# Performance work log

Measured on AMD Instinct MI355X. Metric: run time of the kernel, lower is better.

## Reference

```python
import jax, jax.numpy as jnp
import numpy as np
from jax import lax

BN_EPS = 1e-5


def ternarize(w):
    """Per-output-channel ternary quantization (Li & Liu TWN style).
    delta_i = 0.7 * mean(|w_i|); alpha_i = mean of |w| over entries with |w| > delta_i;
    output = alpha_i * (+1 where w > delta_i, -1 where w < -delta_i, else 0).
    """
    aw = jnp.abs(w)
    axes = tuple(range(1, w.ndim))
    delta = 0.7 * jnp.mean(aw, axis=axes)            # [O]
    d = delta.reshape((-1,) + (1,) * (w.ndim - 1))   # broadcastable
    mask = aw > d
    alpha = jnp.sum(aw * mask, axis=axes) / jnp.sum(mask, axis=axes)
    tern = jnp.where(w > d, 1.0, 0.0) - jnp.where(w < -d, 1.0, 0.0)
    return tern * alpha.reshape(d.shape)


def batchnorm2d(x, gamma, beta):
    # training-mode batchnorm: batch statistics over (N, H, W), biased variance
    mean = jnp.mean(x, axis=(0, 2, 3), keepdims=True)
    var = jnp.mean((x - mean) ** 2, axis=(0, 2, 3), keepdims=True)
    xhat = (x - mean) * lax.rsqrt(var + BN_EPS)
    return xhat * gamma[None, :, None, None] + beta[None, :, None, None]


def conv2d(x, w, b):
    out = lax.conv_general_dilated(x, w, window_strides=(1, 1), padding='VALID',
                                   dimension_numbers=('NCHW', 'OIHW', 'NCHW'))
    return out + b[None, :, None, None]


def maxpool2(x):
    return lax.reduce_window(x, -jnp.inf, lax.max, (1, 1, 2, 2), (1, 1, 2, 2), 'VALID')


def setup_inputs() -> dict:
    key = jax.random.key(0)
    ks = jax.random.split(key, 10)
    B = 4096
    return {
        'x': jax.random.normal(ks[0], (B, 1, 28, 28), jnp.float32),
        'w_conv1': jax.random.normal(ks[1], (32, 1, 5, 5), jnp.float32) * 0.2,
        'b_conv1': jax.random.normal(ks[2], (32,), jnp.float32) * 0.1,
        'gamma1': jnp.ones((32,), jnp.float32),
        'beta1': jnp.zeros((32,), jnp.float32),
        'w_conv2': jax.random.normal(ks[3], (64, 32, 5, 5), jnp.float32) * 0.05,
        'b_conv2': jax.random.normal(ks[4], (64,), jnp.float32) * 0.1,
        'gamma2': jnp.ones((64,), jnp.float32),
        'beta2': jnp.zeros((64,), jnp.float32),
        'w_fc1': jax.random.normal(ks[5], (512, 1024), jnp.float32) * 0.03,
        'b_fc1': jax.random.normal(ks[6], (512,), jnp.float32) * 0.1,
        'w_fc2': jax.random.normal(ks[7], (10, 512), jnp.float32) * 0.05,
        'b_fc2': jax.random.normal(ks[8], (10,), jnp.float32) * 0.1,
    }


def reference(x, w_conv1, b_conv1, gamma1, beta1, w_conv2, b_conv2, gamma2, beta2,
              w_fc1, b_fc1, w_fc2, b_fc2):
    h = conv2d(x, ternarize(w_conv1), b_conv1)          # [B,32,24,24]
    h = jax.nn.relu(maxpool2(batchnorm2d(h, gamma1, beta1)))  # [B,32,12,12]
    h = conv2d(h, ternarize(w_conv2), b_conv2)          # [B,64,8,8]
    h = jax.nn.relu(maxpool2(batchnorm2d(h, gamma2, beta2)))  # [B,64,4,4]
    h = h.reshape(-1, 1024)
    h = jax.nn.relu(h @ ternarize(w_fc1).T + b_fc1)     # [B,512]
    return h @ ternarize(w_fc2).T + b_fc2               # [B,10]
```

## Files before the change

kernel.cpp:

```cpp
#include <hip/hip_runtime.h>

#define TID ((int)threadIdx.x)
typedef unsigned short ushort_t;
typedef short short8 __attribute__((ext_vector_type(8)));
typedef float f32x4 __attribute__((ext_vector_type(4)));

__device__ __forceinline__ float bf2f(ushort_t u) {
    return __uint_as_float(((unsigned int)u) << 16);
}
__device__ __forceinline__ ushort_t f2bf(float f) {
    unsigned int x = __float_as_uint(f);
    return (ushort_t)((x + 0x7FFFu + ((x >> 16) & 1u)) >> 16);
}
__device__ __forceinline__ float ld1(const void* p, int i, bool f32) {
    return f32 ? ((const float*)p)[i] : bf2f(((const ushort_t*)p)[i]);
}
__device__ __forceinline__ bool probe_f32(const void* g1) {
    return ((const ushort_t*)g1)[0] == 0x0000u;
}
__device__ __forceinline__ short8 bn8relu(short8 u, float a, float h) {
    short8 r;
#pragma unroll
    for (int j = 0; j < 8; ++j) {
        float v = bf2f((ushort_t)u[j]);
        r[j] = (short)f2bf(fmaxf(fmaf(a, v, h), 0.f));
    }
    return r;
}

__global__ __launch_bounds__(256) void tern_pack_kernel(
    const void* __restrict__ w1, const void* __restrict__ w2,
    const void* __restrict__ wf1, const void* __restrict__ wf2,
    ushort_t* __restrict__ wpack1, ushort_t* __restrict__ wpack2,
    ushort_t* __restrict__ wf1pack, ushort_t* __restrict__ wf2pack,
    float* __restrict__ stats_z, const void* __restrict__ g1probe)
{
    const bool f32 = probe_f32(g1probe);
    const int blk = blockIdx.x;
    if (blk < 48) stats_z[blk * 256 + TID] = 0.f;

    const void* w; int K, o, seg;
    if (blk < 32)       { w = w1;  K = 25;   o = blk;       seg = 0; }
    else if (blk < 96)  { w = w2;  K = 800;  o = blk - 32;  seg = 1; }
    else if (blk < 608) { w = wf1; K = 1024; o = blk - 96;  seg = 2; }
    else                { w = wf2; K = 512;  o = blk - 608; seg = 3; }

    const size_t base = (size_t)o * K;
    __shared__ float redA[4], redB[4], redC[4];
    const int lane = TID & 63, wv = TID >> 6;

    float wreg[4];
#pragma unroll
    for (int t = 0; t < 4; ++t) {
        const int k = t * 256 + TID;
        wreg[t] = (k < K) ? ld1(w, base + k, f32) : 0.f;
    }

    float s = fabsf(wreg[0]) + fabsf(wreg[1]) + fabsf(wreg[2]) + fabsf(wreg[3]);
#pragma unroll
    for (int d = 1; d < 64; d <<= 1) s += __shfl_xor(s, d);
    if (lane == 0) redA[wv] = s;
    __syncthreads();
    const float delta = 0.7f * (redA[0] + redA[1] + redA[2] + redA[3]) / (float)K;

    float ms = 0.f, cnt = 0.f;
#pragma unroll
    for (int t = 0; t < 4; ++t) {
        float aw = fabsf(wreg[t]);
        if (aw > delta) { ms += aw; cnt += 1.f; }
    }
#pragma unroll
    for (int d = 1; d < 64; d <<= 1) {
        ms += __shfl_xor(ms, d);
        cnt += __shfl_xor(cnt, d);
    }
    if (lane == 0) { redB[wv] = ms; redC[wv] = cnt; }
    __syncthreads();
    const float denom = redC[0] + redC[1] + redC[2] + redC[3];
    const float alpha = (denom > 0.f)
        ? ((redB[0] + redB[1] + redB[2] + redB[3]) / denom) : 0.f;

#pragma unroll
    for (int t = 0; t < 4; ++t) {
        const int k = t * 256 + TID;
        if (k >= K) break;
        float v = wreg[t];
        ushort_t tb = f2bf((v > delta) ? alpha : ((v < -delta) ? -alpha : 0.f));
        if (seg == 0) {
            const int kp = (k / 5) * 6 + (k % 5);
            wpack1[((size_t)(o >> 4) * 64 + (kp >> 3) * 16 + (o & 15)) * 8 + (kp & 7)] = tb;
        } else if (seg == 1) {
            const int pos = k % 25, ic = k / 25;
            wpack2[((size_t)(pos * 4 + (o >> 4)) * 64 + (ic >> 3) * 16 + (o & 15)) * 8
                   + (ic & 7)] = tb;
        } else if (seg == 2) {
            wf1pack[((size_t)((k >> 5) * 32 + (o >> 4)) * 64 + ((k >> 3) & 3) * 16
                     + (o & 15)) * 8 + (k & 7)] = tb;
        } else {
            wf2pack[((size_t)(k >> 5) * 64 + ((k >> 3) & 3) * 16 + o) * 8 + (k & 7)] = tb;
        }
    }
    if (seg == 0 && TID < 7) {
        const int kps[7] = {5, 11, 17, 23, 29, 30, 31};
        const int kp = kps[TID];
        wpack1[((size_t)(o >> 4) * 64 + (kp >> 3) * 16 + (o & 15)) * 8 + (kp & 7)] = 0;
    }
}

__device__ __forceinline__ void conv1_koff(int qd, int* koff) {
#pragma unroll
    for (int j = 0; j < 8; ++j) {
        int k = qd * 8 + j, ky = k / 6, kx = k - ky * 6;
        koff[j] = (k < 30 && kx < 5) ? (ky * 28 + kx) : -1;
    }
}

__global__ __launch_bounds__(256) void conv1_stats_kernel(
    const void* __restrict__ x, const ushort_t* __restrict__ wpack1u,
    const void* __restrict__ gamma1, float* __restrict__ stats,
    ushort_t* __restrict__ pooled1)
{
    const bool f32 = probe_f32(gamma1);
    const short8* wpack1 = (const short8*)wpack1u;
    __shared__ uint xsI[784];
    __shared__ float reds[4][64];
    const int b0 = blockIdx.x * 2;
    if (TID < 196) {
        uint4 u;
        if (f32) {
            float4 v0 = ((const float4*)x)[(size_t)b0 * 196 + TID];
            float4 v1 = ((const float4*)x)[(size_t)(b0 + 1) * 196 + TID];
            u.x = (uint)f2bf(v0.x) | ((uint)f2bf(v1.x) << 16);
            u.y = (uint)f2bf(v0.y) | ((uint)f2bf(v1.y) << 16);
            u.z = (uint)f2bf(v0.z) | ((uint)f2bf(v1.z) << 16);
            u.w = (uint)f2bf(v0.w) | ((uint)f2bf(v1.w) << 16);
        } else {
            ushort4 u0 = ((const ushort4*)x)[(size_t)b0 * 196 + TID];
            ushort4 u1 = ((const ushort4*)x)[(size_t)(b0 + 1) * 196 + TID];
            u.x = (uint)u0.x | ((uint)u1.x << 16);
            u.y = (uint)u0.y | ((uint)u1.y << 16);
            u.z = (uint)u0.z | ((uint)u1.z << 16);
            u.w = (uint)u0.w | ((uint)u1.w << 16);
        }
        *(uint4*)&xsI[TID * 4] = u;
    }
    __syncthreads();

    const int lane = TID & 63, wv = TID >> 6;
    const int qd = lane >> 4, ln15 = lane & 15;
    int koff[8];
    conv1_koff(qd, koff);
    const short8 bw0 = wpack1[lane];
    const short8 bw1 = wpack1[64 + lane];
    const bool pos0 = ld1(gamma1, ln15, f32) >= 0.f;
    const bool pos1 = ld1(gamma1, 16 + ln15, f32) >= 0.f;

    float s0 = 0.f, q0 = 0.f, s1 = 0.f, q1 = 0.f;
    const int cellA0 = (ln15 >> 2);
    const int m3 = ln15 & 3;
    const size_t pbA = (size_t)b0 * 144;
    const size_t pbB = (size_t)(b0 + 1) * 144;
    for (int t = wv * 9; t < wv * 9 + 9; ++t) {
        const int cellA = t * 4 + cellA0;
        const int pbase = ((cellA / 12) * 2 + (m3 >> 1)) * 28
                        + (cellA % 12) * 2 + (m3 & 1);
        uint g[8];
#pragma unroll
        for (int j = 0; j < 8; ++j)
            g[j] = (koff[j] >= 0) ? xsI[pbase + koff[j]] : 0u;
        short8 a0, a1;
#pragma unroll
        for (int j = 0; j < 8; ++j) {
            a0[j] = (short)(g[j] & 0xFFFFu);
            a1[j] = (short)(g[j] >> 16);
        }
        f32x4 c00 = {0.f,0.f,0.f,0.f}, c01 = {0.f,0.f,0.f,0.f};
        f32x4 c10 = {0.f,0.f,0.f,0.f}, c11 = {0.f,0.f,0.f,0.f};
        c00 = __builtin_amdgcn_mfma_f32_16x16x32_bf16(a0, bw0, c00, 0, 0, 0);
        c01 = __builtin_amdgcn_mfma_f32_16x16x32_bf16(a0, bw1, c01, 0, 0, 0);
        c10 = __builtin_amdgcn_mfma_f32_16x16x32_bf16(a1, bw0, c10, 0, 0, 0);
        c11 = __builtin_amdgcn_mfma_f32_16x16x32_bf16(a1, bw1, c11, 0, 0, 0);
#pragma unroll
        for (int r = 0; r < 4; ++r) {
            s0 += c00[r] + c10[r]; q0 += c00[r]*c00[r] + c10[r]*c10[r];
            s1 += c01[r] + c11[r]; q1 += c01[r]*c01[r] + c11[r]*c11[r];
        }
        const int cell = t * 4 + qd;
        float mxA0 = fmaxf(fmaxf(c00[0], c00[1]), fmaxf(c00[2], c00[3]));
        float mnA0 = fminf(fminf(c00[0], c00[1]), fminf(c00[2], c00[3]));
        float mxA1 = fmaxf(fmaxf(c01[0], c01[1]), fmaxf(c01[2], c01[3]));
        float mnA1 = fminf(fminf(c01[0], c01[1]), fminf(c01[2], c01[3]));
        pooled1[(pbA + cell) * 32 + ln15]      = f2bf(pos0 ? mxA0 : mnA0);
        pooled1[(pbA + cell) * 32 + 16 + ln15] = f2bf(pos1 ? mxA1 : mnA1);
        float mxB0 = fmaxf(fmaxf(c10[0], c10[1]), fmaxf(c10[2], c10[3]));
        float mnB0 = fminf(fminf(c10[0], c10[1]), fminf(c10[2], c10[3]));
        float mxB1 = fmaxf(fmaxf(c11[0], c11[1]), fmaxf(c11[2], c11[3]));
        float mnB1 = fminf(fminf(c11[0], c11[1]), fminf(c11[2], c11[3]));
        pooled1[(pbB + cell) * 32 + ln15]      = f2bf(pos0 ? mxB0 : mnB0);
        pooled1[(pbB + cell) * 32 + 16 + ln15] = f2bf(pos1 ? mxB1 : mnB1);
    }
    s0 += __shfl_xor(s0, 16); q0 += __shfl_xor(q0, 16);
    s1 += __shfl_xor(s1, 16); q1 += __shfl_xor(q1, 16);
    s0 += __shfl_xor(s0, 32); q0 += __shfl_xor(q0, 32);
    s1 += __shfl_xor(s1, 32); q1 += __shfl_xor(q1, 32);
    if (lane < 16) {
        reds[wv][ln15]      = s0;
        reds[wv][32 + ln15] = q0;
        reds[wv][16 + ln15] = s1;
        reds[wv][48 + ln15] = q1;
    }
    __syncthreads();
    if (TID < 64) {
        float v = reds[0][TID] + reds[1][TID] + reds[2][TID] + reds[3][TID];
        atomicAdd(&stats[(blockIdx.x & 63) * 64 + TID], v);
    }
}

__global__ __launch_bounds__(256) void conv12_kernel(
    const ushort_t* __restrict__ pooled1, const float* __restrict__ stats,
    const void* __restrict__ gamma1, const void* __restrict__ beta1,
    const ushort_t* __restrict__ wpack2u,
    const void* __restrict__ b2, const void* __restrict__ gamma2,
    ushort_t* __restrict__ pooled2, float* __restrict__ stats2)
{
    const bool f32 = probe_f32(gamma1);
    const short8* wpack2 = (const short8*)wpack2u;
    __shared__ ushort_t p1b[2][144 * 40];
    __shared__ float r2[4][64];
    __shared__ float as1[32], hs1[32];
    const int b0 = blockIdx.x * 2;

    {
        const int c = TID & 63, g = TID >> 6;
        float v = 0.f;
        for (int sl = g; sl < 64; sl += 4) v += stats[sl * 64 + c];
        r2[g][c] = v;
    }
    __syncthreads();
    if (TID < 32) {
        float s = r2[0][TID] + r2[1][TID] + r2[2][TID] + r2[3][TID];
        float q = r2[0][32 + TID] + r2[1][32 + TID]
                + r2[2][32 + TID] + r2[3][32 + TID];
        const float invN = 1.f / 2359296.f;
        float mraw = s * invN;
        float var  = q * invN - mraw * mraw;
        float rstd = rsqrtf(fmaxf(var, 0.f) + 1e-5f);
        float g1v = ld1(gamma1, TID, f32) * rstd;
        as1[TID] = g1v;
        hs1[TID] = ld1(beta1, TID, f32) - mraw * g1v;
    }
    __syncthreads();

    {
        const uint* pm = (const uint*)(pooled1 + (size_t)b0 * 4608);
        const int ch2 = (TID & 15) * 2;
        const float aA = as1[ch2],     hA = hs1[ch2];
        const float aB = as1[ch2 + 1], hB = hs1[ch2 + 1];
#pragma unroll
        for (int i = 0; i < 18; ++i) {
            const int idx = i * 256 + TID;
            const int img = (idx >= 2304) ? 1 : 0;
            const int cell = (idx - img * 2304) >> 4;
            const uint u = pm[idx];
            float v0 = bf2f((ushort_t)(u & 0xFFFFu));
            float v1 = bf2f((ushort_t)(u >> 16));
            uint o0 = f2bf(fmaxf(fmaf(aA, v0, hA), 0.f));
            uint o1 = f2bf(fmaxf(fmaf(aB, v1, hB), 0.f));
            *(uint*)&p1b[img][cell * 40 + ch2] = o0 | (o1 << 16);
        }
    }
    __syncthreads();

    const int lane = TID & 63, wv = TID >> 6;
    const int qd = lane >> 4, ln15 = lane & 15;
    const int mh = wv >> 1, nh = wv & 1;
    const int px0 = (mh * 2 + 0) * 16 + ln15;
    const int px1 = (mh * 2 + 1) * 16 + ln15;
    const int base0 = (px0 >> 3) * 12 + (px0 & 7);
    const int base1 = (px1 >> 3) * 12 + (px1 & 7);

    f32x4 acc[2][2][2] = {};
#pragma unroll
    for (int pos = 0; pos < 25; ++pos) {
        const int koff2 = (pos / 5) * 12 + (pos % 5);
        short8 bb0 = wpack2[(pos * 4 + nh * 2 + 0) * 64 + lane];
        short8 bb1 = wpack2[(pos * 4 + nh * 2 + 1) * 64 + lane];
#pragma unroll
        for (int img = 0; img < 2; ++img) {
            short8 a0 = *(const short8*)&p1b[img][(base0 + koff2) * 40 + qd * 8];
            short8 a1 = *(const short8*)&p1b[img][(base1 + koff2) * 40 + qd * 8];
            acc[img][0][0] = __builtin_amdgcn_mfma_f32_16x16x32_bf16(a0, bb0, acc[img][0][0], 0, 0, 0);
            acc[img][0][1] = __builtin_amdgcn_mfma_f32_16x16x32_bf16(a0, bb1, acc[img][0][1], 0, 0, 0);
            acc[img][1][0] = __builtin_amdgcn_mfma_f32_16x16x32_bf16(a1, bb0, acc[img][1][0], 0, 0, 0);
            acc[img][1][1] = __builtin_amdgcn_mfma_f32_16x16x32_bf16(a1, bb1, acc[img][1][1], 0, 0, 0);
        }
    }

#pragma unroll
    for (int jn = 0; jn < 2; ++jn) {
        const int oc = (nh * 2 + jn) * 16 + ln15;
        const float bias = ld1(b2, oc, f32);
        const bool gpos = ld1(gamma2, oc, f32) >= 0.f;
        float s0 = 0.f, q0 = 0.f;
#pragma unroll
        for (int img = 0; img < 2; ++img) {
            const size_t p2base = (size_t)(b0 + img) * 1024;
#pragma unroll
            for (int i = 0; i < 2; ++i) {
                float v0 = acc[img][i][jn][0] + bias;
                float v1 = acc[img][i][jn][1] + bias;
                float v2 = acc[img][i][jn][2] + bias;
                float v3 = acc[img][i][jn][3] + bias;
                s0 += v0 + v1 + v2 + v3;
                q0 += v0*v0 + v1*v1 + v2*v2 + v3*v3;
                float mx01 = fmaxf(v0, v1), mn01 = fminf(v0, v1);
                float mx23 = fmaxf(v2, v3), mn23 = fminf(v2, v3);
                mx01 = fmaxf(mx01, __shfl_xor(mx01, 32));
                mn01 = fminf(mn01, __shfl_xor(mn01, 32));
                mx23 = fmaxf(mx23, __shfl_xor(mx23, 32));
                mn23 = fminf(mn23, __shfl_xor(mn23, 32));
                if (qd < 2) {
                    ushort2 st;
                    st.x = f2bf(gpos ? mx01 : mn01);
                    st.y = f2bf(gpos ? mx23 : mn23);
                    const int ti = mh * 2 + i;
                    *(ushort2*)&pooled2[p2base + (size_t)oc * 16 + ti * 4 + 2 * qd] = st;
                }
            }
        }
        s0 += __shfl_down(s0, 32); q0 += __shfl_down(q0, 32);
        s0 += __shfl_down(s0, 16); q0 += __shfl_down(q0, 16);
        if (lane < 16) {
            r2[wv][jn * 32 + lane]      = s0;
            r2[wv][jn * 32 + 16 + lane] = q0;
        }
    }
    __syncthreads();
    if (TID < 128) {
        const int idx = TID & 63, nh2 = TID >> 6;
        float v = r2[nh2][idx] + r2[nh2 + 2][idx];
        const int jn = idx >> 5, isq = (idx >> 4) & 1, chx = idx & 15;
        const int oc = nh2 * 32 + jn * 16 + chx;
        atomicAdd(&stats2[(blockIdx.x & 63) * 128 + isq * 64 + oc], v);
    }
}

__global__ __launch_bounds__(256) void fc1_kernel(
    const ushort_t* __restrict__ A, const ushort_t* __restrict__ wf1packu,
    const float* __restrict__ stats2,
    const void* __restrict__ gamma2, const void* __restrict__ beta2,
    const void* __restrict__ bias, ushort_t* __restrict__ out,
    const void* __restrict__ g1probe)
{
    const bool f32 = probe_f32(g1probe);
    const short8* wf1pack = (const short8*)wf1packu;
    __shared__ float bn2[2][128];
    __shared__ float a2s[64], h2s[64];
    const int m0 = blockIdx.y * 64;
    const int n0x4 = blockIdx.x * 4;
    const int lane = TID & 63;
    const int wv   = TID >> 6;
    const int mh = wv >> 1, nh = wv & 1;
    const int qd = lane >> 4, ln15 = lane & 15;

    {
        const int c = TID & 127, g = TID >> 7;
        float v = 0.f;
        for (int sl = g; sl < 64; sl += 2) v += stats2[sl * 128 + c];
        bn2[g][c] = v;
    }
    __syncthreads();
    if (TID < 64) {
        float s = bn2[0][TID] + bn2[1][TID];
        float q = bn2[0][64 + TID] + bn2[1][64 + TID];
        const float invN = 1.f / 262144.f;
        float mean = s * invN;
        float var  = q * invN - mean * mean;
        float rstd = rsqrtf(fmaxf(var, 0.f) + 1e-5f);
        float g2 = ld1(gamma2, TID, f32) * rstd;
        a2s[TID] = g2;
        h2s[TID] = ld1(beta2, TID, f32) - mean * g2;
    }
    __syncthreads();

    const ushort_t* arow0 = A + (size_t)(m0 + mh * 32 + ln15) * 1024 + qd * 8;
    const ushort_t* arow1 = arow0 + 16 * 1024;

    f32x4 acc[2][2] = {};
#pragma unroll 8
    for (int kk = 0; kk < 32; ++kk) {
        const int oc = kk * 2 + (qd >> 1);
        const float a2 = a2s[oc], h2 = h2s[oc];
        short8 a0 = bn8relu(*(const short8*)(arow0 + kk * 32), a2, h2);
        short8 a1 = bn8relu(*(const short8*)(arow1 + kk * 32), a2, h2);
        short8 bb0 = wf1pack[(kk * 32 + n0x4 + nh * 2 + 0) * 64 + lane];
        short8 bb1 = wf1pack[(kk * 32 + n0x4 + nh * 2 + 1) * 64 + lane];
        acc[0][0] = __builtin_amdgcn_mfma_f32_16x16x32_bf16(a0, bb0, acc[0][0], 0, 0, 0);
        acc[0][1] = __builtin_amdgcn_mfma_f32_16x16x32_bf16(a0, bb1, acc[0][1], 0, 0, 0);
        acc[1][0] = __builtin_amdgcn_mfma_f32_16x16x32_bf16(a1, bb0, acc[1][0], 0, 0, 0);
        acc[1][1] = __builtin_amdgcn_mfma_f32_16x16x32_bf16(a1, bb1, acc[1][1], 0, 0, 0);
    }

#pragma unroll
    for (int jn = 0; jn < 2; ++jn) {
        const int n = n0x4 * 16 + (nh * 2 + jn) * 16 + ln15;
        const float bv = ld1(bias, n, f32);
#pragma unroll
        for (int i = 0; i < 2; ++i) {
            const int mb = m0 + (mh * 2 + i) * 16 + qd * 4;
#pragma unroll
            for (int r = 0; r < 4; ++r) {
                float v = fmaxf(acc[i][jn][r] + bv, 0.f);
                out[(size_t)(mb + r) * 512 + n] = f2bf(v);
            }
        }
    }
}

__global__ __launch_bounds__(256) void fc2_kernel(
    const ushort_t* __restrict__ h, const ushort_t* __restrict__ wf2packu,
    const void* __restrict__ bias, void* __restrict__ out,
    const void* __restrict__ g1probe)
{
    const bool f32 = probe_f32(g1probe);
    const short8* wf2pack = (const short8*)wf2packu;
    const int lane = TID & 63, wv = TID >> 6;
    const int qd = lane >> 4, ln15 = lane & 15;
    const int m0 = (blockIdx.x * 4 + wv) * 16;

    f32x4 acc = {0.f, 0.f, 0.f, 0.f};
#pragma unroll
    for (int kk = 0; kk < 16; ++kk) {
        short8 a = *(const short8*)&h[(size_t)(m0 + ln15) * 512 + kk * 32 + qd * 8];
        acc = __builtin_amdgcn_mfma_f32_16x16x32_bf16(a, wf2pack[kk * 64 + lane],
                                                      acc, 0, 0, 0);
    }
    if (ln15 < 10) {
        const float bv = ld1(bias, ln15, f32);
#pragma unroll
        for (int r = 0; r < 4; ++r) {
            const size_t oi = (size_t)(m0 + qd * 4 + r) * 10 + ln15;
            float v = acc[r] + bv;
            if (f32) ((float*)out)[oi] = v;
            else ((ushort_t*)out)[oi] = f2bf(v);
        }
    }
}

extern "C" void kernel_launch(void* const* d_in, const int* in_sizes, int n_in,
                              void* d_out, int out_size, void* d_ws, size_t ws_size,
                              hipStream_t stream)
{
    const void* x       = d_in[0];
    const void* w_conv1 = d_in[1];
    const void* gamma1  = d_in[3];
    const void* beta1   = d_in[4];
    const void* w_conv2 = d_in[5];
    const void* b_conv2 = d_in[6];
    const void* gamma2  = d_in[7];
    const void* beta2   = d_in[8];
    const void* w_fc1   = d_in[9];
    const void* b_fc1   = d_in[10];
    const void* w_fc2   = d_in[11];
    const void* b_fc2   = d_in[12];

    char* wsb = (char*)d_ws;
    size_t off = 0;
    auto alloc = [&](size_t bytes) -> void* {
        void* p = wsb + off;
        off += (bytes + 255) & ~(size_t)255;
        return p;
    };

    float*    stats   = (float*)alloc(49152);
    float*    stats2  = stats + 4096;
    ushort_t* wpack1  = (ushort_t*)alloc(2 * 64 * 16);
    ushort_t* wpack2  = (ushort_t*)alloc(25 * 4 * 64 * 16);
    ushort_t* wf1pack = (ushort_t*)alloc((size_t)32 * 32 * 64 * 16);
    ushort_t* wf2pack = (ushort_t*)alloc(16 * 64 * 16);
    ushort_t* pooled1 = (ushort_t*)alloc((size_t)4096 * 144 * 32 * 2);
    ushort_t* pooled2 = (ushort_t*)alloc((size_t)4096 * 64 * 16 * 2);
    ushort_t* fc1o    = (ushort_t*)alloc((size_t)4096 * 512 * 2);

    tern_pack_kernel<<<618, 256, 0, stream>>>(w_conv1, w_conv2, w_fc1, w_fc2,
                                              wpack1, wpack2, wf1pack, wf2pack,
                                              stats, gamma1);

    conv1_stats_kernel<<<2048, 256, 0, stream>>>(x, wpack1, gamma1,
                                                 stats, pooled1);

    conv12_kernel<<<2048, 256, 0, stream>>>(pooled1, stats, gamma1, beta1,
                                            wpack2, b_conv2, gamma2,
                                            pooled2, stats2);

    fc1_kernel<<<dim3(8, 64), 256, 0, stream>>>(pooled2, wf1pack, stats2,
                                                gamma2, beta2, b_fc1,
                                                fc1o, gamma1);
    fc2_kernel<<<64, 256, 0, stream>>>(fc1o, wf2pack, b_fc2, d_out, gamma1);
}
```

Before: 182.2 us.

## Recompute conv1 in conv2 kernel instead of materializing pooled1

The conv1 kernel now only computes batch statistics. The conv2 kernel reloads the input image, recomputes conv1 with MFMA, and applies BN, maxpool and ReLU directly into shared memory. This removes the global write and read of the large pooled1 intermediate, about 75 MB of bf16 traffic. The cost is doing the conv1 MFMAs twice and adding extra shared memory for the input tile in the conv2 kernel.

```diff
diff --git a/kernel.cpp b/kernel.cpp
--- a/kernel.cpp
+++ b/kernel.cpp
@@ -114,17 +114,8 @@
         koff[j] = (k < 30 && kx < 5) ? (ky * 28 + kx) : -1;
     }
 }
-
-__global__ __launch_bounds__(256) void conv1_stats_kernel(
-    const void* __restrict__ x, const ushort_t* __restrict__ wpack1u,
-    const void* __restrict__ gamma1, float* __restrict__ stats,
-    ushort_t* __restrict__ pooled1)
-{
-    const bool f32 = probe_f32(gamma1);
-    const short8* wpack1 = (const short8*)wpack1u;
-    __shared__ uint xsI[784];
-    __shared__ float reds[4][64];
-    const int b0 = blockIdx.x * 2;
+__device__ __forceinline__ void load_x2(const void* x, int b0, bool f32,
+                                        uint* xsI) {
     if (TID < 196) {
         uint4 u;
         if (f32) {
@@ -144,6 +135,18 @@
         }
         *(uint4*)&xsI[TID * 4] = u;
     }
+}
+
+__global__ __launch_bounds__(256) void conv1_stats_kernel(
+    const void* __restrict__ x, const ushort_t* __restrict__ wpack1u,
+    const void* __restrict__ gamma1, float* __restrict__ stats)
+{
+    const bool f32 = probe_f32(gamma1);
+    const short8* wpack1 = (const short8*)wpack1u;
+    __shared__ uint xsI[784];
+    __shared__ float reds[4][64];
+    const int b0 = blockIdx.x * 2;
+    load_x2(x, b0, f32, xsI);
     __syncthreads();
 
     const int lane = TID & 63, wv = TID >> 6;
@@ -152,14 +155,10 @@
     conv1_koff(qd, koff);
     const short8 bw0 = wpack1[lane];
     const short8 bw1 = wpack1[64 + lane];
-    const bool pos0 = ld1(gamma1, ln15, f32) >= 0.f;
-    const bool pos1 = ld1(gamma1, 16 + ln15, f32) >= 0.f;
 
     float s0 = 0.f, q0 = 0.f, s1 = 0.f, q1 = 0.f;
     const int cellA0 = (ln15 >> 2);
     const int m3 = ln15 & 3;
-    const size_t pbA = (size_t)b0 * 144;
-    const size_t pbB = (size_t)(b0 + 1) * 144;
     for (int t = wv * 9; t < wv * 9 + 9; ++t) {
         const int cellA = t * 4 + cellA0;
         const int pbase = ((cellA / 12) * 2 + (m3 >> 1)) * 28
@@ -185,19 +184,6 @@
             s0 += c00[r] + c10[r]; q0 += c00[r]*c00[r] + c10[r]*c10[r];
             s1 += c01[r] + c11[r]; q1 += c01[r]*c01[r] + c11[r]*c11[r];
         }
-        const int cell = t * 4 + qd;
-        float mxA0 = fmaxf(fmaxf(c00[0], c00[1]), fmaxf(c00[2], c00[3]));
-        float mnA0 = fminf(fminf(c00[0], c00[1]), fminf(c00[2], c00[3]));
-        float mxA1 = fmaxf(fmaxf(c01[0], c01[1]), fmaxf(c01[2], c01[3]));
-        float mnA1 = fminf(fminf(c01[0], c01[1]), fminf(c01[2], c01[3]));
-        pooled1[(pbA + cell) * 32 + ln15]      = f2bf(pos0 ? mxA0 : mnA0);
-        pooled1[(pbA + cell) * 32 + 16 + ln15] = f2bf(pos1 ? mxA1 : mnA1);
-        float mxB0 = fmaxf(fmaxf(c10[0], c10[1]), fmaxf(c10[2], c10[3]));
-        float mnB0 = fminf(fminf(c10[0], c10[1]), fminf(c10[2], c10[3]));
-        float mxB1 = fmaxf(fmaxf(c11[0], c11[1]), fmaxf(c11[2], c11[3]));
-        float mnB1 = fminf(fminf(c11[0], c11[1]), fminf(c11[2], c11[3]));
-        pooled1[(pbB + cell) * 32 + ln15]      = f2bf(pos0 ? mxB0 : mnB0);
-        pooled1[(pbB + cell) * 32 + 16 + ln15] = f2bf(pos1 ? mxB1 : mnB1);
     }
     s0 += __shfl_xor(s0, 16); q0 += __shfl_xor(q0, 16);
     s1 += __shfl_xor(s1, 16); q1 += __shfl_xor(q1, 16);
@@ -217,19 +203,22 @@
 }
 
 __global__ __launch_bounds__(256) void conv12_kernel(
-    const ushort_t* __restrict__ pooled1, const float* __restrict__ stats,
+    const void* __restrict__ x, const float* __restrict__ stats,
     const void* __restrict__ gamma1, const void* __restrict__ beta1,
-    const ushort_t* __restrict__ wpack2u,
+    const ushort_t* __restrict__ wpack1u, const ushort_t* __restrict__ wpack2u,
     const void* __restrict__ b2, const void* __restrict__ gamma2,
     ushort_t* __restrict__ pooled2, float* __restrict__ stats2)
 {
     const bool f32 = probe_f32(gamma1);
+    const short8* wpack1 = (const short8*)wpack1u;
     const short8* wpack2 = (const short8*)wpack2u;
+    __shared__ uint xsI[784];
     __shared__ ushort_t p1b[2][144 * 40];
     __shared__ float r2[4][64];
     __shared__ float as1[32], hs1[32];
     const int b0 = blockIdx.x * 2;
 
+    load_x2(x, b0, f32, xsI);
     {
         const int c = TID & 63, g = TID >> 6;
         float v = 0.f;
@@ -251,28 +240,56 @@
     }
     __syncthreads();
 
-    {
-        const uint* pm = (const uint*)(pooled1 + (size_t)b0 * 4608);
-        const int ch2 = (TID & 15) * 2;
-        const float aA = as1[ch2],     hA = hs1[ch2];
-        const float aB = as1[ch2 + 1], hB = hs1[ch2 + 1];
-#pragma unroll
-        for (int i = 0; i < 18; ++i) {
-            const int idx = i * 256 + TID;
-            const int img = (idx >= 2304) ? 1 : 0;
-            const int cell = (idx - img * 2304) >> 4;
-            const uint u = pm[idx];
-            float v0 = bf2f((ushort_t)(u & 0xFFFFu));
-            float v1 = bf2f((ushort_t)(u >> 16));
-            uint o0 = f2bf(fmaxf(fmaf(aA, v0, hA), 0.f));
-            uint o1 = f2bf(fmaxf(fmaf(aB, v1, hB), 0.f));
-            *(uint*)&p1b[img][cell * 40 + ch2] = o0 | (o1 << 16);
-        }
-    }
-    __syncthreads();
-
     const int lane = TID & 63, wv = TID >> 6;
     const int qd = lane >> 4, ln15 = lane & 15;
+
+    {
+        int koff[8];
+        conv1_koff(qd, koff);
+        const short8 bw0 = wpack1[lane];
+        const short8 bw1 = wpack1[64 + lane];
+        const float g0 = as1[ln15],      h0 = hs1[ln15];
+        const float g1 = as1[16 + ln15], h1 = hs1[16 + ln15];
+        const int cellA0 = (ln15 >> 2);
+        const int m3 = ln15 & 3;
+        for (int t = wv * 9; t < wv * 9 + 9; ++t) {
+            const int cellA = t * 4 + cellA0;
+            const int pbase = ((cellA / 12) * 2 + (m3 >> 1)) * 28
+                            + (cellA % 12) * 2 + (m3 & 1);
+            uint g[8];
+#pragma unroll
+            for (int j = 0; j < 8; ++j)
+                g[j] = (koff[j] >= 0) ? xsI[pbase + koff[j]] : 0u;
+            short8 a0, a1;
+#pragma unroll
+            for (int j = 0; j < 8; ++j) {
+                a0[j] = (short)(g[j] & 0xFFFFu);
+                a1[j] = (short)(g[j] >> 16);
+            }
+            f32x4 c00 = {0.f,0.f,0.f,0.f}, c01 = {0.f,0.f,0.f,0.f};
+            f32x4 c10 = {0.f,0.f,0.f,0.f}, c11 = {0.f,0.f,0.f,0.f};
+            c00 = __builtin_amdgcn_mfma_f32_16x16x32_bf16(a0, bw0, c00, 0, 0, 0);
+            c01 = __builtin_amdgcn_mfma_f32_16x16x32_bf16(a0, bw1, c01, 0, 0, 0);
+            c10 = __builtin_amdgcn_mfma_f32_16x16x32_bf16(a1, bw0, c10, 0, 0, 0);
+            c11 = __builtin_amdgcn_mfma_f32_16x16x32_bf16(a1, bw1, c11, 0, 0, 0);
+            const int cell = t * 4 + qd;
+            float m00 = fmaf(c00[0], g0, h0), m01 = fmaf(c01[0], g1, h1);
+            float m10 = fmaf(c10[0], g0, h0), m11 = fmaf(c11[0], g1, h1);
+#pragma unroll
+            for (int r = 1; r < 4; ++r) {
+                m00 = fmaxf(m00, fmaf(c00[r], g0, h0));
+                m01 = fmaxf(m01, fmaf(c01[r], g1, h1));
+                m10 = fmaxf(m10, fmaf(c10[r], g0, h0));
+                m11 = fmaxf(m11, fmaf(c11[r], g1, h1));
+            }
+            p1b[0][cell * 40 + ln15]      = f2bf(fmaxf(m00, 0.f));
+            p1b[0][cell * 40 + 16 + ln15] = f2bf(fmaxf(m01, 0.f));
+            p1b[1][cell * 40 + ln15]      = f2bf(fmaxf(m10, 0.f));
+            p1b[1][cell * 40 + 16 + ln15] = f2bf(fmaxf(m11, 0.f));
+        }
+    }
+    __syncthreads();
+
     const int mh = wv >> 1, nh = wv & 1;
     const int px0 = (mh * 2 + 0) * 16 + ln15;
     const int px1 = (mh * 2 + 1) * 16 + ln15;
@@ -478,7 +495,6 @@
     ushort_t* wpack2  = (ushort_t*)alloc(25 * 4 * 64 * 16);
     ushort_t* wf1pack = (ushort_t*)alloc((size_t)32 * 32 * 64 * 16);
     ushort_t* wf2pack = (ushort_t*)alloc(16 * 64 * 16);
-    ushort_t* pooled1 = (ushort_t*)alloc((size_t)4096 * 144 * 32 * 2);
     ushort_t* pooled2 = (ushort_t*)alloc((size_t)4096 * 64 * 16 * 2);
     ushort_t* fc1o    = (ushort_t*)alloc((size_t)4096 * 512 * 2);
 
@@ -486,11 +502,10 @@
                                               wpack1, wpack2, wf1pack, wf2pack,
                                               stats, gamma1);
 
-    conv1_stats_kernel<<<2048, 256, 0, stream>>>(x, wpack1, gamma1,
-                                                 stats, pooled1);
-
-    conv12_kernel<<<2048, 256, 0, stream>>>(pooled1, stats, gamma1, beta1,
-                                            wpack2, b_conv2, gamma2,
+    conv1_stats_kernel<<<2048, 256, 0, stream>>>(x, wpack1, gamma1, stats);
+
+    conv12_kernel<<<2048, 256, 0, stream>>>(x, stats, gamma1, beta1,
+                                            wpack1, wpack2, b_conv2, gamma2,
                                             pooled2, stats2);
 
     fc1_kernel<<<dim3(8, 64), 256, 0, stream>>>(pooled2, wf1pack, stats2,
```

After: 197.0 us. +8.2%, slower.
